# Kernel tuning notes

Hardware: AMD Instinct MI355X
Metric: run time of the kernel (lower is better)

## Reference

```python
import jax, jax.numpy as jnp
import numpy as np

N, L, D = 2, 2048, 1024
H, KV, HD = 16, 4, 64
CAP = 50.0


def _rope_cache(L, hd):
    inv_freq = 1.0 / (10000.0 ** (np.arange(0, hd, 2, dtype=np.float32) / hd))
    t = np.arange(L, dtype=np.float32)
    freqs = np.outer(t, inv_freq)                      # (L, hd/2)
    emb = np.concatenate([freqs, freqs], axis=-1)      # (L, hd)
    return jnp.asarray(np.cos(emb)), jnp.asarray(np.sin(emb))


def setup_inputs() -> dict:
    key = jax.random.key(0)
    ks = jax.random.split(key, 6)
    s = 0.02
    cos, sin = _rope_cache(L, HD)
    return {
        "x": jax.random.normal(ks[0], (N, L, D), jnp.float32),
        "Wq": jax.random.normal(ks[1], (D, H * HD), jnp.float32) * s,
        "bq": jnp.zeros((H * HD,), jnp.float32),
        "Wk": jax.random.normal(ks[2], (D, KV * HD), jnp.float32) * s,
        "bk": jnp.zeros((KV * HD,), jnp.float32),
        "Wv": jax.random.normal(ks[3], (D, KV * HD), jnp.float32) * s,
        "bv": jnp.zeros((KV * HD,), jnp.float32),
        "Wo": jax.random.normal(ks[4], (D, D), jnp.float32) * s,
        "bo": jnp.zeros((D,), jnp.float32),
        "q_gamma": jnp.ones((H, HD), jnp.float32),
        "k_gamma": jnp.ones((KV, HD), jnp.float32),
        "rope_cos": cos,
        "rope_sin": sin,
        "is_causal": 1,
    }


def _rmsnorm(t, gamma):
    # t: (N, heads, L, HD); gamma: (heads, HD)
    inv = jax.lax.rsqrt(jnp.mean(t * t, axis=-1, keepdims=True) + 1e-6)
    return t * inv * gamma[None, :, None, :]


def _apply_rope(t, cos, sin):
    # t: (N, heads, L, HD); cos/sin: (L, HD)
    hd = t.shape[-1]
    t1, t2 = t[..., : hd // 2], t[..., hd // 2:]
    rot = jnp.concatenate([-t2, t1], axis=-1)
    return t * cos[None, None] + rot * sin[None, None]


def reference(x, Wq, bq, Wk, bk, Wv, bv, Wo, bo, q_gamma, k_gamma, rope_cos, rope_sin, is_causal):
    n, l, d = x.shape
    h, hd = q_gamma.shape
    kv = k_gamma.shape[0]
    n_rep = h // kv

    q = (x @ Wq + bq).reshape(n, l, h, hd).transpose(0, 2, 1, 3)   # (n,h,l,hd)
    k = (x @ Wk + bk).reshape(n, l, kv, hd).transpose(0, 2, 1, 3)  # (n,kv,l,hd)
    v = (x @ Wv + bv).reshape(n, l, kv, hd).transpose(0, 2, 1, 3)

    q = _rmsnorm(q, q_gamma)
    k = _rmsnorm(k, k_gamma)
    q = _apply_rope(q, rope_cos, rope_sin)
    k = _apply_rope(k, rope_cos, rope_sin)

    if n_rep > 1:
        k = jnp.repeat(k, n_rep, axis=1)
        v = jnp.repeat(v, n_rep, axis=1)

    scale = hd ** -0.5
    logits = jnp.einsum("bhqd,bhkd->bhqk", q, k) * scale
    logits = CAP * jnp.tanh(logits / CAP)
    if is_causal:
        causal = jnp.tril(jnp.ones((l, l), dtype=bool))
        logits = jnp.where(causal[None, None], logits, -jnp.inf)
    weights = jax.nn.softmax(logits, axis=-1)
    y = jnp.einsum("bhqk,bhkd->bhqd", weights, v)
    y = y.transpose(0, 2, 1, 3).reshape(n, l, d)
    return y @ Wo + bo
```

## Files before the change

### kernel.cpp

```cpp
#include <hip/hip_runtime.h>
#include <hip/hip_bf16.h>

typedef __attribute__((ext_vector_type(8))) short short8;
typedef __attribute__((ext_vector_type(4))) float f32x4;
typedef __attribute__((ext_vector_type(4))) unsigned int u32x4;

using bf16 = __hip_bfloat16;

#define L_SEQ 2048
#define NB 2
#define DM 1024
#define NH 16
#define NKV 4
#define HDIM 64
#define CAPV 50.0f

#if __has_builtin(__builtin_amdgcn_exp2f)
#define EXP2(x) __builtin_amdgcn_exp2f(x)
#else
#define EXP2(x) exp2f(x)
#endif

__device__ __forceinline__ unsigned short f2bs(float f) {
  bf16 h = __float2bfloat16(f);
  return __builtin_bit_cast(unsigned short, h);
}

__device__ __forceinline__ float bs2f(unsigned short u) {
  return __bfloat162float(__builtin_bit_cast(bf16, u));
}

__device__ __forceinline__ unsigned int cvt_pk_bf16(float lo, float hi) {
  unsigned int w;
  asm("v_cvt_pk_bf16_f32 %0, %1, %2" : "=v"(w) : "v"(lo), "v"(hi));
  return w;
}

__device__ __forceinline__ void gload_lds16(const void* g, void* l) {
  __builtin_amdgcn_global_load_lds(
      (const __attribute__((address_space(1))) void*)g,
      (__attribute__((address_space(3))) void*)l, 16, 0, 0);
}

__global__ void k_cvt_x(const float* __restrict__ x, ushort* __restrict__ xb) {
  int i = (blockIdx.x * blockDim.x + threadIdx.x) * 4;
  float4 v = *reinterpret_cast<const float4*>(x + i);
  ushort4 o = make_ushort4(f2bs(v.x), f2bs(v.y), f2bs(v.z), f2bs(v.w));
  *reinterpret_cast<ushort4*>(xb + i) = o;
}

__global__ void k_transpose_all(const float* __restrict__ Wq, const float* __restrict__ Wk,
                                const float* __restrict__ Wv, const float* __restrict__ Wo,
                                bf16* __restrict__ wqt, bf16* __restrict__ wkt,
                                bf16* __restrict__ wvt, bf16* __restrict__ wot) {
  __shared__ float tile[32][33];
  const int z = blockIdx.z;
  const float* W = (z == 0) ? Wq : (z == 1) ? Wk : (z == 2) ? Wv : Wo;
  bf16* Wt = (z == 0) ? wqt : (z == 1) ? wkt : (z == 2) ? wvt : wot;
  const int Ncols = (z == 1 || z == 2) ? 256 : 1024;
  const int bx = blockIdx.x * 32;
  if (bx >= Ncols) return;
  const int by = blockIdx.y * 32;
  const int tx = threadIdx.x, ty = threadIdx.y;
  #pragma unroll
  for (int j = 0; j < 32; j += 8)
    tile[ty + j][tx] = W[(size_t)(by + ty + j) * Ncols + bx + tx];
  __syncthreads();
  #pragma unroll
  for (int j = 0; j < 32; j += 8)
    Wt[(size_t)(bx + ty + j) * 1024 + by + tx] = __float2bfloat16(tile[tx][ty + j]);
}

template<int OUT_MODE>
__global__ __launch_bounds__(256) void k_gemm(const bf16* __restrict__ A,
                                              const bf16* __restrict__ Bt,
                                              const float* __restrict__ bq,
                                              const float* __restrict__ bk,
                                              const float* __restrict__ bv,
                                              const float* __restrict__ qg,
                                              const float* __restrict__ kg,
                                              const float* __restrict__ rcT,
                                              const float* __restrict__ rsT,
                                              void* __restrict__ out0,
                                              void* __restrict__ out1,
                                              void* __restrict__ out2,
                                              int M, int Ncols, int K) {
  __shared__ __align__(16) bf16 As[2][64 * 64];
  __shared__ __align__(16) bf16 Bs[2][128 * 64];
  const int t = threadIdx.x;
  const int lane = t & 63;
  const int w = t >> 6;
  const int wr = w >> 1, wc = w & 1;
  const int m0 = blockIdx.y * 64, n0 = blockIdx.x * 128;
  const int lr = lane & 15, lg = lane >> 4;
  const int nkt = K >> 6;

  f32x4 acc[2][4];
  #pragma unroll
  for (int m = 0; m < 2; ++m)
    #pragma unroll
    for (int n = 0; n < 4; ++n)
      acc[m][n] = f32x4{0.f, 0.f, 0.f, 0.f};

  {
    #pragma unroll
    for (int p = 0; p < 2; ++p) {
      const int Gb = p * 256 + w * 64;
      const int G = Gb + lane;
      const int row = G >> 3, gc = G & 7;
      gload_lds16(&A[(size_t)(m0 + row) * K + ((gc ^ (row & 7)) * 8)], &As[0][Gb * 8]);
    }
    #pragma unroll
    for (int p = 0; p < 4; ++p) {
      const int Gb = p * 256 + w * 64;
      const int G = Gb + lane;
      const int row = G >> 3, gc = G & 7;
      gload_lds16(&Bt[(size_t)(n0 + row) * K + ((gc ^ (row & 7)) * 8)], &Bs[0][Gb * 8]);
    }
  }
  int cur = 0;

  for (int kt = 0; kt < nkt; ++kt) {
    __syncthreads();

    if (kt + 1 < nkt) {
      const int kofs = (kt + 1) * 64;
      #pragma unroll
      for (int p = 0; p < 2; ++p) {
        const int Gb = p * 256 + w * 64;
        const int G = Gb + lane;
        const int row = G >> 3, gc = G & 7;
        gload_lds16(&A[(size_t)(m0 + row) * K + kofs + ((gc ^ (row & 7)) * 8)],
                    &As[cur ^ 1][Gb * 8]);
      }
      #pragma unroll
      for (int p = 0; p < 4; ++p) {
        const int Gb = p * 256 + w * 64;
        const int G = Gb + lane;
        const int row = G >> 3, gc = G & 7;
        gload_lds16(&Bt[(size_t)(n0 + row) * K + kofs + ((gc ^ (row & 7)) * 8)],
                    &Bs[cur ^ 1][Gb * 8]);
      }
    }

    #pragma unroll
    for (int ks = 0; ks < 2; ++ks) {
      short8 af[2], bfr[4];
      #pragma unroll
      for (int m = 0; m < 2; ++m) {
        const int row = wr * 32 + m * 16 + lr;
        af[m] = *reinterpret_cast<const short8*>(
            &As[cur][row * 64 + (((ks * 4 + lg) ^ (row & 7)) * 8)]);
      }
      #pragma unroll
      for (int n = 0; n < 4; ++n) {
        const int row = wc * 64 + n * 16 + lr;
        bfr[n] = *reinterpret_cast<const short8*>(
            &Bs[cur][row * 64 + (((ks * 4 + lg) ^ (row & 7)) * 8)]);
      }
      #pragma unroll
      for (int m = 0; m < 2; ++m)
        #pragma unroll
        for (int n = 0; n < 4; ++n)
          acc[m][n] = __builtin_amdgcn_mfma_f32_16x16x32_bf16(af[m], bfr[n], acc[m][n], 0, 0, 0);
    }
    cur ^= 1;
  }

  const int colbase = n0 + wc * 64;

  if (OUT_MODE == 1) {
    #pragma unroll
    for (int m = 0; m < 2; ++m) {
      const int row = m0 + wr * 32 + m * 16 + lg * 4;
      #pragma unroll
      for (int n = 0; n < 4; ++n) {
        const int col = colbase + n * 16 + lr;
        const float bvv = bq[col];
        #pragma unroll
        for (int r = 0; r < 4; ++r)
          reinterpret_cast<float*>(out0)[(size_t)(row + r) * Ncols + col] = acc[m][n][r] + bvv;
      }
    }
  } else {
    if (colbase >= 1280) {
      #pragma unroll
      for (int m = 0; m < 2; ++m) {
        const int row = m0 + wr * 32 + m * 16 + lg * 4;
        const int bb = row >> 11, l = row & 2047;
        #pragma unroll
        for (int n = 0; n < 4; ++n) {
          const int d = colbase - 1280 + n * 16 + lr;
          const float bvv = bv[d];
          ushort4 o;
          o.x = f2bs(acc[m][n][0] + bvv);
          o.y = f2bs(acc[m][n][1] + bvv);
          o.z = f2bs(acc[m][n][2] + bvv);
          o.w = f2bs(acc[m][n][3] + bvv);
          *reinterpret_cast<ushort4*>(
              &reinterpret_cast<bf16*>(out2)[((size_t)bb * 256 + d) * L_SEQ + l]) = o;
        }
      }
    } else {
      const bool isQ = (colbase < 1024);
      const float* bias = isQ ? bq : bk;
      const float* gma = isQ ? qg : kg;
      bf16* dst0 = reinterpret_cast<bf16*>(isQ ? out0 : out1);
      const int cb = isQ ? colbase : (colbase - 1024);
      const int head = cb >> 6;
      const int heads = isQ ? NH : NKV;
      float g[4];
      #pragma unroll
      for (int n = 0; n < 4; ++n) g[n] = gma[cb + n * 16 + lr];
      #pragma unroll
      for (int m = 0; m < 2; ++m) {
        const int row = m0 + wr * 32 + m * 16 + lg * 4;
        float vv[4][4];
        float ss[4] = {0.f, 0.f, 0.f, 0.f};
        #pragma unroll
        for (int n = 0; n < 4; ++n) {
          const float bvv = bias[cb + n * 16 + lr];
          #pragma unroll
          for (int r = 0; r < 4; ++r) {
            vv[n][r] = acc[m][n][r] + bvv;
            ss[r] = fmaf(vv[n][r], vv[n][r], ss[r]);
          }
        }
        #pragma unroll
        for (int r = 0; r < 4; ++r) {
          float s = ss[r];
          s += __shfl_xor(s, 1, 64);
          s += __shfl_xor(s, 2, 64);
          s += __shfl_xor(s, 4, 64);
          s += __shfl_xor(s, 8, 64);
          ss[r] = rsqrtf(s * (1.0f / 64.0f) + 1e-6f);
        }
        float tv[4][4];
        #pragma unroll
        for (int n = 0; n < 4; ++n)
          #pragma unroll
          for (int r = 0; r < 4; ++r)
            tv[n][r] = vv[n][r] * ss[r] * g[n];
        #pragma unroll
        for (int r = 0; r < 4; ++r) {
          const int grow = row + r;
          const int bb = grow >> 11, l = grow & 2047;
          bf16* dst = dst0 + (((size_t)bb * heads + head) * L_SEQ + l) * HDIM;
          #pragma unroll
          for (int n = 0; n < 4; ++n) {
            const int d = n * 16 + lr;
            const float c = rcT[l * HDIM + d];
            const float s2 = rsT[l * HDIM + d];
            const float rot = (n < 2) ? -tv[n ^ 2][r] : tv[n ^ 2][r];
            dst[d] = __float2bfloat16(fmaf(tv[n][r], c, rot * s2));
          }
        }
      }
    }
  }
}

__global__ __launch_bounds__(256) void k_attn(
    const bf16* __restrict__ qb, const bf16* __restrict__ kb,
    const bf16* __restrict__ vt, bf16* __restrict__ y,
    bf16* __restrict__ pO, float* __restrict__ pd,
    const int* __restrict__ causal_flag) {
  __shared__ __align__(16) bf16 Ks[2][64 * 64];
  __shared__ __align__(16) bf16 Vs[2][64 * 64];

  const int t = threadIdx.x, lane = t & 63, w = t >> 6;
  const int lr = lane & 15, lg = lane >> 4;
  const int jx = blockIdx.x;
  const int bh = blockIdx.y;
  const int half = blockIdx.z;
  const int b = bh >> 4, h = bh & 15;
  const int kvh = h >> 2;
  const bool causal = (*causal_flag) != 0;

  const int T_a = causal ? (2 * jx + 2) : 32;
  const int T_b = causal ? (32 - 2 * jx) : 32;
  const int total = T_a + T_b;
  const int mid = (total + 1) >> 1;
  const int g0 = half ? mid : 0;
  const int g1 = half ? total : mid;

  const bf16* kbase = kb + ((size_t)b * NKV + kvh) * L_SEQ * HDIM;
  const bf16* vbase = vt + ((size_t)b * NKV + kvh) * HDIM * L_SEQ;

  for (int seg = 0; seg < 2; ++seg) {
    const int qp = seg ? (15 - jx) : jx;
    const int ts = seg ? T_b : T_a;
    const int base = seg ? T_a : 0;
    const int lo = max(0, g0 - base);
    const int hi = min(ts, g1 - base);
    if (lo >= hi) continue;

    const int q0 = qp * 128;
    const int wrow = q0 + w * 32;

    short8 qf[2][2];
    #pragma unroll
    for (int s = 0; s < 2; ++s) {
      const bf16* qrow = qb + (((size_t)bh) * L_SEQ + wrow + s * 16 + lr) * HDIM;
      qf[s][0] = *reinterpret_cast<const short8*>(qrow + lg * 8);
      qf[s][1] = *reinterpret_cast<const short8*>(qrow + 32 + lg * 8);
    }

    f32x4 o0[4], o1[4];
    #pragma unroll
    for (int n = 0; n < 4; ++n) {
      o0[n] = f32x4{0.f, 0.f, 0.f, 0.f};
      o1[n] = f32x4{0.f, 0.f, 0.f, 0.f};
    }
    float plt0 = 0.f, plt1 = 0.f;

    __syncthreads();
    {
      const int k00 = lo * 64;
      #pragma unroll
      for (int i = 0; i < 2; ++i) {
        const int Gb = i * 256 + w * 64;
        const int G = Gb + lane;
        const int row = G >> 3, gc = G & 7;
        gload_lds16(kbase + (size_t)(k00 + row) * HDIM + ((gc ^ (row & 7)) * 8), &Ks[0][Gb * 8]);
        gload_lds16(vbase + (size_t)row * L_SEQ + k00 + ((gc ^ (row & 7)) * 8), &Vs[0][Gb * 8]);
      }
    }
    int cur = 0;

    for (int kt = lo; kt < hi; ++kt) {
      __syncthreads();

      if (kt + 1 < hi) {
        const int k0n = (kt + 1) * 64;
        #pragma unroll
        for (int i = 0; i < 2; ++i) {
          const int Gb = i * 256 + w * 64;
          const int G = Gb + lane;
          const int row = G >> 3, gc = G & 7;
          gload_lds16(kbase + (size_t)(k0n + row) * HDIM + ((gc ^ (row & 7)) * 8),
                      &Ks[cur ^ 1][Gb * 8]);
          gload_lds16(vbase + (size_t)row * L_SEQ + k0n + ((gc ^ (row & 7)) * 8),
                      &Vs[cur ^ 1][Gb * 8]);
        }
      }

      f32x4 s0[4], s1[4];
      #pragma unroll
      for (int n = 0; n < 4; ++n) {
        s0[n] = f32x4{0.f, 0.f, 0.f, 0.f};
        s1[n] = f32x4{0.f, 0.f, 0.f, 0.f};
      }
      #pragma unroll
      for (int n = 0; n < 4; ++n) {
        const int krow = n * 16 + lr;
        short8 kf0 = *reinterpret_cast<const short8*>(
            &Ks[cur][krow * 64 + ((lg ^ (krow & 7)) * 8)]);
        short8 kf1 = *reinterpret_cast<const short8*>(
            &Ks[cur][krow * 64 + (((4 + lg) ^ (krow & 7)) * 8)]);
        s0[n] = __builtin_amdgcn_mfma_f32_16x16x32_bf16(kf0, qf[0][0], s0[n], 0, 0, 0);
        s0[n] = __builtin_amdgcn_mfma_f32_16x16x32_bf16(kf1, qf[0][1], s0[n], 0, 0, 0);
        s1[n] = __builtin_amdgcn_mfma_f32_16x16x32_bf16(kf0, qf[1][0], s1[n], 0, 0, 0);
        s1[n] = __builtin_amdgcn_mfma_f32_16x16x32_bf16(kf1, qf[1][1], s1[n], 0, 0, 0);
      }

      const int k0 = kt * 64;
      #pragma unroll
      for (int n = 0; n < 4; ++n) {
        #pragma unroll
        for (int r = 0; r < 4; ++r) {
          float xs = s0[n][r];
          s0[n][r] = fmaf(xs * 0.18033688f, fmaf(xs * xs, -2.0833333e-6f, 1.0f), -16.0f);
          xs = s1[n][r];
          s1[n][r] = fmaf(xs * 0.18033688f, fmaf(xs * xs, -2.0833333e-6f, 1.0f), -16.0f);
        }
      }
      if (causal && (k0 + 63 > wrow)) {
        #pragma unroll
        for (int n = 0; n < 4; ++n) {
          const int keyb = k0 + n * 16 + lg * 4;
          #pragma unroll
          for (int r = 0; r < 4; ++r)
            if (keyb + r > wrow + lr) s0[n][r] = -1e30f;
        }
      }
      if (causal && (k0 + 63 > wrow + 16)) {
        #pragma unroll
        for (int n = 0; n < 4; ++n) {
          const int keyb = k0 + n * 16 + lg * 4;
          #pragma unroll
          for (int r = 0; r < 4; ++r)
            if (keyb + r > wrow + 16 + lr) s1[n][r] = -1e30f;
        }
      }

      unsigned int w0[8], w1[8];
      #pragma unroll
      for (int n = 0; n < 4; ++n) {
        const float a0 = EXP2(s0[n][0]);
        const float a1 = EXP2(s0[n][1]);
        const float a2 = EXP2(s0[n][2]);
        const float a3 = EXP2(s0[n][3]);
        plt0 += (a0 + a1) + (a2 + a3);
        w0[2 * n] = cvt_pk_bf16(a0, a1);
        w0[2 * n + 1] = cvt_pk_bf16(a2, a3);
        const float c0 = EXP2(s1[n][0]);
        const float c1 = EXP2(s1[n][1]);
        const float c2 = EXP2(s1[n][2]);
        const float c3 = EXP2(s1[n][3]);
        plt1 += (c0 + c1) + (c2 + c3);
        w1[2 * n] = cvt_pk_bf16(c0, c1);
        w1[2 * n + 1] = cvt_pk_bf16(c2, c3);
      }
      short8 pf0[2], pf1[2];
      #pragma unroll
      for (int ks = 0; ks < 2; ++ks) {
        u32x4 a = {w0[4 * ks], w0[4 * ks + 1], w0[4 * ks + 2], w0[4 * ks + 3]};
        u32x4 c = {w1[4 * ks], w1[4 * ks + 1], w1[4 * ks + 2], w1[4 * ks + 3]};
        pf0[ks] = __builtin_bit_cast(short8, a);
        pf1[ks] = __builtin_bit_cast(short8, c);
      }

      const int voff = 4 * (lg & 1);
      #pragma unroll
      for (int ks = 0; ks < 2; ++ks) {
        const int gA = 4 * ks + (lg >> 1);
        #pragma unroll
        for (int n = 0; n < 4; ++n) {
          const int vd = n * 16 + lr;
          const int vb_ = vd * 64;
          const int sw = vd & 7;
          const uint2 vlo = *reinterpret_cast<const uint2*>(
              &Vs[cur][vb_ + ((gA ^ sw) * 8 + voff)]);
          const uint2 vhi = *reinterpret_cast<const uint2*>(
              &Vs[cur][vb_ + (((gA + 2) ^ sw) * 8 + voff)]);
          u32x4 vv = {vlo.x, vlo.y, vhi.x, vhi.y};
          short8 vfr = __builtin_bit_cast(short8, vv);
          o0[n] = __builtin_amdgcn_mfma_f32_16x16x32_bf16(pf0[ks], vfr, o0[n], 0, 0, 0);
          o1[n] = __builtin_amdgcn_mfma_f32_16x16x32_bf16(pf1[ks], vfr, o1[n], 0, 0, 0);
        }
      }
      cur ^= 1;
    }

    const bool full = (lo == 0) && (hi == ts);
    #pragma unroll
    for (int s = 0; s < 2; ++s) {
      float ls = s ? plt1 : plt0;
      ls += __shfl_xor(ls, 16, 64);
      ls += __shfl_xor(ls, 32, 64);
      const f32x4* oa = s ? o1 : o0;
      if (full) {
        #pragma unroll
        for (int r = 0; r < 4; ++r) {
          const float den = __shfl(ls, lg * 4 + r, 64);
          const float invl = __builtin_amdgcn_rcpf(den);
          const int qg_ = wrow + s * 16 + lg * 4 + r;
          #pragma unroll
          for (int n = 0; n < 4; ++n)
            y[((size_t)b * L_SEQ + qg_) * DM + h * HDIM + n * 16 + lr] =
                __float2bfloat16(oa[n][r] * invl);
        }
      } else {
        if (lane < 16)
          pd[((size_t)half * NB * NH + bh) * L_SEQ + wrow + s * 16 + lane] = ls;
        #pragma unroll
        for (int r = 0; r < 4; ++r) {
          const int qg_ = wrow + s * 16 + lg * 4 + r;
          #pragma unroll
          for (int n = 0; n < 4; ++n)
            pO[(((size_t)half * NB + b) * L_SEQ + qg_) * DM + h * HDIM + n * 16 + lr] =
                __float2bfloat16(oa[n][r]);
        }
      }
    }
  }
}

__global__ __launch_bounds__(256) void k_combine(const bf16* __restrict__ pO,
                                                 const float* __restrict__ pd,
                                                 bf16* __restrict__ y,
                                                 const int* __restrict__ causal_flag) {
  if ((*causal_flag) == 0) return;
  const int b = blockIdx.x >> 10;
  const int l = 1024 + (blockIdx.x & 1023);
  const int c4 = threadIdx.x * 4;
  const int h = c4 >> 6;
  const float d0 = pd[((size_t)b * NH + h) * L_SEQ + l];
  const float d1 = pd[((size_t)NB * NH + b * NH + h) * L_SEQ + l];
  const float inv = __builtin_amdgcn_rcpf(d0 + d1);
  const size_t base0 = ((size_t)b * L_SEQ + l) * DM + c4;
  const size_t base1 = (((size_t)NB + b) * L_SEQ + l) * DM + c4;
  ushort4 a = *reinterpret_cast<const ushort4*>(reinterpret_cast<const ushort*>(pO) + base0);
  ushort4 bb = *reinterpret_cast<const ushort4*>(reinterpret_cast<const ushort*>(pO) + base1);
  ushort4 o;
  o.x = f2bs((bs2f(a.x) + bs2f(bb.x)) * inv);
  o.y = f2bs((bs2f(a.y) + bs2f(bb.y)) * inv);
  o.z = f2bs((bs2f(a.z) + bs2f(bb.z)) * inv);
  o.w = f2bs((bs2f(a.w) + bs2f(bb.w)) * inv);
  *reinterpret_cast<ushort4*>(reinterpret_cast<ushort*>(y) +
                              ((size_t)b * L_SEQ + l) * DM + c4) = o;
}

extern "C" void kernel_launch(void* const* d_in, const int* in_sizes, int n_in,
                              void* d_out, int out_size, void* d_ws, size_t ws_size,
                              hipStream_t stream) {
  (void)in_sizes; (void)n_in; (void)out_size; (void)ws_size;
  const float* x  = (const float*)d_in[0];
  const float* Wq = (const float*)d_in[1];
  const float* bq = (const float*)d_in[2];
  const float* Wk = (const float*)d_in[3];
  const float* bk = (const float*)d_in[4];
  const float* Wv = (const float*)d_in[5];
  const float* bv = (const float*)d_in[6];
  const float* Wo = (const float*)d_in[7];
  const float* bo = (const float*)d_in[8];
  const float* qg = (const float*)d_in[9];
  const float* kg = (const float*)d_in[10];
  const float* rc = (const float*)d_in[11];
  const float* rs = (const float*)d_in[12];
  const int* causal = (const int*)d_in[13];
  float* out = (float*)d_out;

  char* ws = (char*)d_ws;
  size_t off = 0;
  auto alloc = [&](size_t bytes) -> char* {
    char* p = ws + off;
    off += (bytes + 255) & ~(size_t)255;
    return p;
  };
  bf16* xb    = (bf16*)alloc((size_t)4096 * 1024 * 2);
  bf16* wqkvt = (bf16*)alloc((size_t)1536 * 1024 * 2);
  bf16* wot   = (bf16*)alloc((size_t)1024 * 1024 * 2);
  bf16* vt    = (bf16*)alloc((size_t)NB * NKV * HDIM * L_SEQ * 2);
  bf16* qb    = (bf16*)alloc((size_t)NB * NH * L_SEQ * HDIM * 2);
  bf16* kb    = (bf16*)alloc((size_t)NB * NKV * L_SEQ * HDIM * 2);
  bf16* y     = (bf16*)alloc((size_t)4096 * 1024 * 2);
  bf16* pO    = (bf16*)alloc((size_t)2 * NB * L_SEQ * DM * 2);
  float* pd   = (float*)alloc((size_t)2 * NB * NH * L_SEQ * 4);
  bf16* wqt   = wqkvt;
  bf16* wkt   = wqkvt + (size_t)1024 * 1024;
  bf16* wvt   = wqkvt + (size_t)1280 * 1024;

  k_cvt_x<<<4096, 256, 0, stream>>>(x, (ushort*)xb);
  k_transpose_all<<<dim3(32, 32, 4), dim3(32, 8), 0, stream>>>(Wq, Wk, Wv, Wo, wqt, wkt, wvt, wot);

  k_gemm<6><<<dim3(12, 64), 256, 0, stream>>>(xb, wqkvt, bq, bk, bv, qg, kg, rc, rs,
                                              qb, kb, vt, 4096, 1536, 1024);

  k_attn<<<dim3(8, NB * NH, 2), 256, 0, stream>>>(qb, kb, vt, y, pO, pd, causal);
  k_combine<<<NB * 1024, 256, 0, stream>>>(pO, pd, y, causal);

  k_gemm<1><<<dim3(8, 64), 256, 0, stream>>>(y, wot, bo, nullptr, nullptr, nullptr, nullptr,
                                             nullptr, nullptr, out, nullptr, nullptr,
                                             4096, 1024, 1024);
}
```

Measured before the change: 96.06 us.

## Fuse split-KV attention combine into output projection GEMM A-tile load

Removes the separate combine kernel and instead merges the two partial attention outputs and denominators while loading the A operand of the Wo GEMM for rows in the second half of the sequence. Those blocks load through registers, normalize, pack to bf16 and write to LDS, overlapping the global loads with MFMA work. This saves a kernel launch and a full write-then-read of y for half the rows. In exchange, heavy blocks do more ALU work, hold more registers and lose the direct global-to-LDS load path, and each partial tile is re-read by all 8 column blocks instead of once.

```diff
diff --git a/kernel.cpp b/kernel.cpp
--- a/kernel.cpp
+++ b/kernel.cpp
@@ -84,6 +84,7 @@
                                               void* __restrict__ out0,
                                               void* __restrict__ out1,
                                               void* __restrict__ out2,
+                                              const int* __restrict__ causal_flag,
                                               int M, int Ncols, int K) {
   __shared__ __align__(16) bf16 As[2][64 * 64];
   __shared__ __align__(16) bf16 Bs[2][128 * 64];
@@ -95,6 +96,17 @@
   const int lr = lane & 15, lg = lane >> 4;
   const int nkt = K >> 6;
 
+  bool heavy = false;
+  const bf16* pO0 = nullptr;
+  const bf16* pO1 = nullptr;
+  const float* pdp = nullptr;
+  if (OUT_MODE == 1) {
+    heavy = ((*causal_flag) != 0) && ((m0 & 1024) != 0);
+    pO0 = reinterpret_cast<const bf16*>(out1);
+    pO1 = pO0 + (size_t)NB * L_SEQ * DM;
+    pdp = reinterpret_cast<const float*>(out2);
+  }
+
   f32x4 acc[2][4];
   #pragma unroll
   for (int m = 0; m < 2; ++m)
@@ -102,47 +114,63 @@
     for (int n = 0; n < 4; ++n)
       acc[m][n] = f32x4{0.f, 0.f, 0.f, 0.f};
 
-  {
+  short8 ra[2], rb[2];
+  float rinv[2];
+  auto issueA = [&](int kofs) {
+    #pragma unroll
+    for (int p = 0; p < 2; ++p) {
+      const int G = p * 256 + w * 64 + lane;
+      const int row = G >> 3, gc = G & 7;
+      const int scol = kofs + ((gc ^ (row & 7)) * 8);
+      const int grow = m0 + row;
+      const int bb = grow >> 11, l = grow & 2047;
+      const size_t base = ((size_t)bb * L_SEQ + l) * DM + scol;
+      ra[p] = *reinterpret_cast<const short8*>(pO0 + base);
+      rb[p] = *reinterpret_cast<const short8*>(pO1 + base);
+      const int hh = scol >> 6;
+      const float d0 = pdp[((size_t)bb * NH + hh) * L_SEQ + l];
+      const float d1 = pdp[(size_t)(NB * NH) * L_SEQ + ((size_t)bb * NH + hh) * L_SEQ + l];
+      rinv[p] = __builtin_amdgcn_rcpf(d0 + d1);
+    }
+  };
+  auto writeA = [&](int buf) {
+    #pragma unroll
+    for (int p = 0; p < 2; ++p) {
+      const int G = p * 256 + w * 64 + lane;
+      const ushort* pa = reinterpret_cast<const ushort*>(&ra[p]);
+      const ushort* pb = reinterpret_cast<const ushort*>(&rb[p]);
+      unsigned int wo[4];
+      #pragma unroll
+      for (int i = 0; i < 4; ++i) {
+        const float lo = (bs2f(pa[2 * i]) + bs2f(pb[2 * i])) * rinv[p];
+        const float hi = (bs2f(pa[2 * i + 1]) + bs2f(pb[2 * i + 1])) * rinv[p];
+        wo[i] = cvt_pk_bf16(lo, hi);
+      }
+      u32x4 pk = {wo[0], wo[1], wo[2], wo[3]};
+      *reinterpret_cast<short8*>(&As[buf][G * 8]) = __builtin_bit_cast(short8, pk);
+    }
+  };
+  auto gloadA = [&](int buf, int kofs) {
     #pragma unroll
     for (int p = 0; p < 2; ++p) {
       const int Gb = p * 256 + w * 64;
       const int G = Gb + lane;
       const int row = G >> 3, gc = G & 7;
-      gload_lds16(&A[(size_t)(m0 + row) * K + ((gc ^ (row & 7)) * 8)], &As[0][Gb * 8]);
-    }
+      gload_lds16(&A[(size_t)(m0 + row) * K + kofs + ((gc ^ (row & 7)) * 8)],
+                  &As[buf][Gb * 8]);
+    }
+  };
+  auto gloadB = [&](int buf, int kofs) {
     #pragma unroll
     for (int p = 0; p < 4; ++p) {
       const int Gb = p * 256 + w * 64;
       const int G = Gb + lane;
       const int row = G >> 3, gc = G & 7;
-      gload_lds16(&Bt[(size_t)(n0 + row) * K + ((gc ^ (row & 7)) * 8)], &Bs[0][Gb * 8]);
-    }
-  }
-  int cur = 0;
-
-  for (int kt = 0; kt < nkt; ++kt) {
-    __syncthreads();
-
-    if (kt + 1 < nkt) {
-      const int kofs = (kt + 1) * 64;
-      #pragma unroll
-      for (int p = 0; p < 2; ++p) {
-        const int Gb = p * 256 + w * 64;
-        const int G = Gb + lane;
-        const int row = G >> 3, gc = G & 7;
-        gload_lds16(&A[(size_t)(m0 + row) * K + kofs + ((gc ^ (row & 7)) * 8)],
-                    &As[cur ^ 1][Gb * 8]);
-      }
-      #pragma unroll
-      for (int p = 0; p < 4; ++p) {
-        const int Gb = p * 256 + w * 64;
-        const int G = Gb + lane;
-        const int row = G >> 3, gc = G & 7;
-        gload_lds16(&Bt[(size_t)(n0 + row) * K + kofs + ((gc ^ (row & 7)) * 8)],
-                    &Bs[cur ^ 1][Gb * 8]);
-      }
-    }
-
+      gload_lds16(&Bt[(size_t)(n0 + row) * K + kofs + ((gc ^ (row & 7)) * 8)],
+                  &Bs[buf][Gb * 8]);
+    }
+  };
+  auto mfmaStep = [&](int buf) {
     #pragma unroll
     for (int ks = 0; ks < 2; ++ks) {
       short8 af[2], bfr[4];
@@ -150,13 +178,13 @@
       for (int m = 0; m < 2; ++m) {
         const int row = wr * 32 + m * 16 + lr;
         af[m] = *reinterpret_cast<const short8*>(
-            &As[cur][row * 64 + (((ks * 4 + lg) ^ (row & 7)) * 8)]);
+            &As[buf][row * 64 + (((ks * 4 + lg) ^ (row & 7)) * 8)]);
       }
       #pragma unroll
       for (int n = 0; n < 4; ++n) {
         const int row = wc * 64 + n * 16 + lr;
         bfr[n] = *reinterpret_cast<const short8*>(
-            &Bs[cur][row * 64 + (((ks * 4 + lg) ^ (row & 7)) * 8)]);
+            &Bs[buf][row * 64 + (((ks * 4 + lg) ^ (row & 7)) * 8)]);
       }
       #pragma unroll
       for (int m = 0; m < 2; ++m)
@@ -164,7 +192,35 @@
         for (int n = 0; n < 4; ++n)
           acc[m][n] = __builtin_amdgcn_mfma_f32_16x16x32_bf16(af[m], bfr[n], acc[m][n], 0, 0, 0);
     }
-    cur ^= 1;
+  };
+
+  int cur = 0;
+  if (OUT_MODE == 1 && heavy) {
+    issueA(0);
+    writeA(0);
+    gloadB(0, 0);
+    for (int kt = 0; kt < nkt; ++kt) {
+      __syncthreads();
+      if (kt + 1 < nkt) {
+        issueA((kt + 1) * 64);
+        gloadB(cur ^ 1, (kt + 1) * 64);
+      }
+      mfmaStep(cur);
+      if (kt + 1 < nkt) writeA(cur ^ 1);
+      cur ^= 1;
+    }
+  } else {
+    gloadA(0, 0);
+    gloadB(0, 0);
+    for (int kt = 0; kt < nkt; ++kt) {
+      __syncthreads();
+      if (kt + 1 < nkt) {
+        gloadA(cur ^ 1, (kt + 1) * 64);
+        gloadB(cur ^ 1, (kt + 1) * 64);
+      }
+      mfmaStep(cur);
+      cur ^= 1;
+    }
   }
 
   const int colbase = n0 + wc * 64;
@@ -475,31 +531,6 @@
       }
     }
   }
-}
-
-__global__ __launch_bounds__(256) void k_combine(const bf16* __restrict__ pO,
-                                                 const float* __restrict__ pd,
-                                                 bf16* __restrict__ y,
-                                                 const int* __restrict__ causal_flag) {
-  if ((*causal_flag) == 0) return;
-  const int b = blockIdx.x >> 10;
-  const int l = 1024 + (blockIdx.x & 1023);
-  const int c4 = threadIdx.x * 4;
-  const int h = c4 >> 6;
-  const float d0 = pd[((size_t)b * NH + h) * L_SEQ + l];
-  const float d1 = pd[((size_t)NB * NH + b * NH + h) * L_SEQ + l];
-  const float inv = __builtin_amdgcn_rcpf(d0 + d1);
-  const size_t base0 = ((size_t)b * L_SEQ + l) * DM + c4;
-  const size_t base1 = (((size_t)NB + b) * L_SEQ + l) * DM + c4;
-  ushort4 a = *reinterpret_cast<const ushort4*>(reinterpret_cast<const ushort*>(pO) + base0);
-  ushort4 bb = *reinterpret_cast<const ushort4*>(reinterpret_cast<const ushort*>(pO) + base1);
-  ushort4 o;
-  o.x = f2bs((bs2f(a.x) + bs2f(bb.x)) * inv);
-  o.y = f2bs((bs2f(a.y) + bs2f(bb.y)) * inv);
-  o.z = f2bs((bs2f(a.z) + bs2f(bb.z)) * inv);
-  o.w = f2bs((bs2f(a.w) + bs2f(bb.w)) * inv);
-  *reinterpret_cast<ushort4*>(reinterpret_cast<ushort*>(y) +
-                              ((size_t)b * L_SEQ + l) * DM + c4) = o;
 }
 
 extern "C" void kernel_launch(void* const* d_in, const int* in_sizes, int n_in,
@@ -546,12 +577,11 @@
   k_transpose_all<<<dim3(32, 32, 4), dim3(32, 8), 0, stream>>>(Wq, Wk, Wv, Wo, wqt, wkt, wvt, wot);
 
   k_gemm<6><<<dim3(12, 64), 256, 0, stream>>>(xb, wqkvt, bq, bk, bv, qg, kg, rc, rs,
-                                              qb, kb, vt, 4096, 1536, 1024);
+                                              qb, kb, vt, causal, 4096, 1536, 1024);
 
   k_attn<<<dim3(8, NB * NH, 2), 256, 0, stream>>>(qb, kb, vt, y, pO, pd, causal);
-  k_combine<<<NB * 1024, 256, 0, stream>>>(pO, pd, y, causal);
 
   k_gemm<1><<<dim3(8, 64), 256, 0, stream>>>(y, wot, bo, nullptr, nullptr, nullptr, nullptr,
-                                             nullptr, nullptr, out, nullptr, nullptr,
+                                             nullptr, nullptr, out, pO, pd, causal,
                                              4096, 1024, 1024);
 }
```

Result: no change. 95.83 us (-0.2%).
